# Optimization experiments

Measured on AMD Instinct MI355X. Metric: run time of the kernel, lower is better.

Reference implementation:

```python
import jax, jax.numpy as jnp
import numpy as np

E, S, B, D, F = 8, 2048, 4, 1024, 4096  # experts, seq, batch, d_model, d_ff


def setup_inputs() -> dict:
    key = jax.random.key(0)
    k_x, k_w1, k_w2, k_m = jax.random.split(key, 4)
    scale = 0.02
    x = jax.random.normal(k_x, (S, B, D), dtype=jnp.float32)
    W1 = jax.random.normal(k_w1, (E, D, F), dtype=jnp.float32) * scale
    b1 = jnp.zeros((E, F), dtype=jnp.float32)
    W2 = jax.random.normal(k_w2, (E, F, D), dtype=jnp.float32) * scale
    b2 = jnp.zeros((E, D), dtype=jnp.float32)
    mask = jax.random.randint(k_m, (S, B), 0, E)  # per-token expert id
    return {"x": x, "W1": W1, "b1": b1, "W2": W2, "b2": b2, "mask": mask}


def reference(x, W1, b1, W2, b2, mask):
    # Eval path of ThorFNN: dense all-expert 2-layer FFN, then per-token
    # random expert mask multiply-sum combine. Dropout is identity in eval.
    # h: [E, S, B, F]
    h = jax.nn.relu(jnp.einsum('sbd,edf->esbf', x, W1) + b1[:, None, None, :])
    # out: [E, S, B, D]
    out = jnp.einsum('esbf,efd->esbd', h, W2) + b2[:, None, None, :]
    sel = (mask[None, :, :, None] == jnp.arange(W1.shape[0])[:, None, None, None]).astype(out.dtype)
    return (out * sel).sum(axis=0)  # [S, B, D]
```

## Files before the change

kernel.cpp:

```cpp
#include <hip/hip_runtime.h>
#include <hip/hip_bf16.h>
#include <stdint.h>

#define E_   8
#define S_   2048
#define B_   4
#define D_   1024
#define F_   4096
#define NTOK (S_ * B_)
#define MAXT 72

typedef __attribute__((ext_vector_type(8))) __bf16 bf16x8;
typedef __attribute__((ext_vector_type(4))) float  f32x4;

#define WS_LIST 4096
#define WS_XB   65536
#define WS_W1T  (WS_XB + 16777216)
#define WS_W2T  WS_W1T
#define WS_H    (WS_W1T + 67108864)

__device__ __forceinline__ void gload_lds16(const void* g, void* l) {
    __builtin_amdgcn_global_load_lds(
        (const __attribute__((address_space(1))) void*)g,
        (__attribute__((address_space(3))) void*)l, 16, 0, 0);
}

__global__ void build_lists(const int* __restrict__ mask,
                            int* __restrict__ meta, int* __restrict__ list) {
    __shared__ int cnt[E_], cur[E_];
    int tid = threadIdx.x;
    if (tid < E_) cnt[tid] = 0;
    __syncthreads();
    for (int t = tid; t < NTOK; t += 256) atomicAdd(&cnt[mask[t]], 1);
    __syncthreads();
    if (tid == 0) {
        int acc = 0, nt = 0;
        for (int e = 0; e < E_; ++e) {
            meta[e] = cnt[e];
            meta[8 + e] = acc;
            cur[e] = acc;
            acc += cnt[e];
        }
        for (int e = 0; e < E_; ++e) {
            int mt = (cnt[e] + 127) >> 7;
            for (int m = 0; m < mt; ++m) meta[32 + nt++] = (e << 16) | m;
        }
        meta[16] = nt;
        for (; nt < MAXT; ++nt) meta[32 + nt] = -1;
    }
    __syncthreads();
    for (int t = tid; t < NTOK; t += 256) {
        int e = mask[t];
        int pos = atomicAdd(&cur[e], 1);
        list[pos] = t;
    }
}

__global__ void convert_x_kernel(const float* __restrict__ x,
                                 __hip_bfloat16* __restrict__ xb) {
    size_t i = ((size_t)blockIdx.x * blockDim.x + threadIdx.x) * 4;
    const float4 v = *(const float4*)(x + i);
    union { __hip_bfloat16 h[4]; uint2 u; } o;
    o.h[0] = __float2bfloat16(v.x);
    o.h[1] = __float2bfloat16(v.y);
    o.h[2] = __float2bfloat16(v.z);
    o.h[3] = __float2bfloat16(v.w);
    *(uint2*)(xb + i) = o.u;
}

__global__ void transpose_convert(const float* __restrict__ src,
                                  __hip_bfloat16* __restrict__ dst,
                                  int R, int C) {
    __shared__ float tile[32][33];
    size_t off = (size_t)blockIdx.z * R * C;
    src += off; dst += off;
    int c0 = blockIdx.x * 32, r0 = blockIdx.y * 32;
    int tx = threadIdx.x & 31, ty = threadIdx.x >> 5;
#pragma unroll
    for (int i = 0; i < 4; ++i)
        tile[ty + 8 * i][tx] = src[(size_t)(r0 + ty + 8 * i) * C + c0 + tx];
    __syncthreads();
#pragma unroll
    for (int i = 0; i < 4; ++i)
        dst[(size_t)(c0 + ty + 8 * i) * R + r0 + tx] =
            __float2bfloat16(tile[tx][ty + 8 * i]);
}

template <int KDIM, int NDIM, int LAYER>
__global__ __launch_bounds__(256, 2) void gemm_kernel(
    const uint8_t* __restrict__ Abase,
    const uint8_t* __restrict__ Wt,
    const float* __restrict__ bias,
    const int* __restrict__ meta, const int* __restrict__ list,
    __hip_bfloat16* __restrict__ Hout, float* __restrict__ Oout) {
    int te = meta[32 + blockIdx.x];
    if (te < 0) return;
    const int e = te >> 16, mt = te & 0xffff;
    const int cnt = meta[e], bse = meta[8 + e];
    const int n0 = blockIdx.y * 128;
    const int tid = threadIdx.x, wv = tid >> 6, l = tid & 63;
    const int wr = wv >> 1, wc = wv & 1;

    __shared__ __align__(16) uint8_t smem[2][32768];

    const uint8_t* WtE = Wt + (size_t)e * NDIM * KDIM * 2;

    size_t agoff[4], bgoff[4];
#pragma unroll
    for (int p = 0; p < 4; ++p) {
        int r = p * 32 + wv * 8 + (l >> 3);
        int grow = mt * 128 + r;
        int pidx = bse + (grow < cnt ? grow : cnt - 1);
        size_t arow = (LAYER == 1) ? (size_t)list[pidx] : (size_t)pidx;
        agoff[p] = arow * (KDIM * 2) + (size_t)(l & 7) * 16;
        bgoff[p] = (size_t)(n0 + r) * (KDIM * 2) + (size_t)(l & 7) * 16;
    }

    f32x4 acc[4][4] = {};

    auto stage = [&](int buf, int kt) {
        uint8_t* As = &smem[buf][0];
        uint8_t* Bs = &smem[buf][16384];
        size_t kb = (size_t)kt * 128;
#pragma unroll
        for (int p = 0; p < 4; ++p) {
            gload_lds16(Abase + agoff[p] + kb, As + (p * 32 + wv * 8) * 128);
            gload_lds16(WtE + bgoff[p] + kb, Bs + (p * 32 + wv * 8) * 128);
        }
    };

    auto compute = [&](int buf) {
        const uint8_t* As = &smem[buf][0];
        const uint8_t* Bs = &smem[buf][16384];
#pragma unroll
        for (int ks = 0; ks < 2; ++ks) {
            bf16x8 a[4], b[4];
#pragma unroll
            for (int mi = 0; mi < 4; ++mi)
                a[mi] = *(const bf16x8*)(As +
                    ((wr * 64 + mi * 16 + (l & 15)) * 64 + ks * 32 + (l >> 4) * 8) * 2);
#pragma unroll
            for (int ni = 0; ni < 4; ++ni)
                b[ni] = *(const bf16x8*)(Bs +
                    ((wc * 64 + ni * 16 + (l & 15)) * 64 + ks * 32 + (l >> 4) * 8) * 2);
#pragma unroll
            for (int mi = 0; mi < 4; ++mi)
#pragma unroll
                for (int ni = 0; ni < 4; ++ni)
                    acc[mi][ni] = __builtin_amdgcn_mfma_f32_16x16x32_bf16(
                        a[mi], b[ni], acc[mi][ni], 0, 0, 0);
        }
    };

    const int KT = KDIM / 64;
    stage(0, 0);
    __syncthreads();
    int cur = 0;
    for (int kt = 0; kt < KT - 1; ++kt) {
        stage(cur ^ 1, kt + 1);
        compute(cur);
        __syncthreads();
        cur ^= 1;
    }
    compute(cur);

#pragma unroll
    for (int mi = 0; mi < 4; ++mi) {
#pragma unroll
        for (int i = 0; i < 4; ++i) {
            int rl = wr * 64 + mi * 16 + (l >> 4) * 4 + i;
            int grow = mt * 128 + rl;
            if (grow < cnt) {
#pragma unroll
                for (int ni = 0; ni < 4; ++ni) {
                    int col = n0 + wc * 64 + ni * 16 + (l & 15);
                    float v = acc[mi][ni][i] + bias[(size_t)e * NDIM + col];
                    if (LAYER == 1) {
                        v = fmaxf(v, 0.f);
                        Hout[(size_t)(bse + grow) * NDIM + col] = __float2bfloat16(v);
                    } else {
                        int tok = list[bse + grow];
                        Oout[(size_t)tok * NDIM + col] = v;
                    }
                }
            }
        }
    }
}

extern "C" void kernel_launch(void* const* d_in, const int* in_sizes, int n_in,
                              void* d_out, int out_size, void* d_ws, size_t ws_size,
                              hipStream_t stream) {
    const float* x  = (const float*)d_in[0];
    const float* W1 = (const float*)d_in[1];
    const float* b1 = (const float*)d_in[2];
    const float* W2 = (const float*)d_in[3];
    const float* b2 = (const float*)d_in[4];
    const int* mask = (const int*)d_in[5];
    float* out = (float*)d_out;

    uint8_t* ws = (uint8_t*)d_ws;
    int* meta = (int*)ws;
    int* list = (int*)(ws + WS_LIST);
    __hip_bfloat16* xb  = (__hip_bfloat16*)(ws + WS_XB);
    __hip_bfloat16* w1t = (__hip_bfloat16*)(ws + WS_W1T);
    __hip_bfloat16* w2t = (__hip_bfloat16*)(ws + WS_W2T);
    __hip_bfloat16* H   = (__hip_bfloat16*)(ws + WS_H);

    build_lists<<<1, 256, 0, stream>>>(mask, meta, list);
    convert_x_kernel<<<NTOK * D_ / 4 / 256, 256, 0, stream>>>(x, xb);
    transpose_convert<<<dim3(F_ / 32, D_ / 32, E_), 256, 0, stream>>>(W1, w1t, D_, F_);
    gemm_kernel<D_, F_, 1><<<dim3(MAXT, F_ / 128), 256, 0, stream>>>(
        (const uint8_t*)xb, (const uint8_t*)w1t, b1, meta, list, H, nullptr);
    transpose_convert<<<dim3(D_ / 32, F_ / 32, E_), 256, 0, stream>>>(W2, w2t, F_, D_);
    gemm_kernel<F_, D_, 2><<<dim3(MAXT, D_ / 128), 256, 0, stream>>>(
        (const uint8_t*)H, (const uint8_t*)w2t, b2, meta, list, nullptr, out);
}
```

Measured before the change: 612.1 us.

## Shrink GEMM K-tile, raise occupancy, swizzle blocks per XCD, widen transpose

The GEMM now stages K in 32-element slices instead of 64, halving LDS use per block, and launch bounds go from 2 to 4 blocks per CU for higher occupancy. The 2D grid is flattened and remapped so that consecutive tiles of the same expert land on the same XCD, improving L2 reuse of weights. The weight transpose-convert uses 128-row tiles with float4 loads and 8-byte bf16 stores to cut memory transactions. The smaller K-step doubles the number of barriers per tile, and the 4-block launch bound may force register spilling with 64 accumulator floats per thread.

```diff
diff --git a/kernel.cpp b/kernel.cpp
--- a/kernel.cpp
+++ b/kernel.cpp
@@ -71,88 +71,105 @@
 __global__ void transpose_convert(const float* __restrict__ src,
                                   __hip_bfloat16* __restrict__ dst,
                                   int R, int C) {
-    __shared__ float tile[32][33];
+    __shared__ float tile[128][33];
     size_t off = (size_t)blockIdx.z * R * C;
-    src += off; dst += off;
-    int c0 = blockIdx.x * 32, r0 = blockIdx.y * 32;
-    int tx = threadIdx.x & 31, ty = threadIdx.x >> 5;
-#pragma unroll
-    for (int i = 0; i < 4; ++i)
-        tile[ty + 8 * i][tx] = src[(size_t)(r0 + ty + 8 * i) * C + c0 + tx];
-    __syncthreads();
-#pragma unroll
-    for (int i = 0; i < 4; ++i)
-        dst[(size_t)(c0 + ty + 8 * i) * R + r0 + tx] =
-            __float2bfloat16(tile[tx][ty + 8 * i]);
+    const float* s = src + off;
+    __hip_bfloat16* d = dst + off;
+    int r0 = blockIdx.y * 128, c0 = blockIdx.x * 32;
+    int t = threadIdx.x;
+    int rr = t >> 3, cc4 = (t & 7) * 4;
+#pragma unroll
+    for (int ii = 0; ii < 4; ++ii) {
+        float4 v = *(const float4*)(s + (size_t)(r0 + rr + 32 * ii) * C + c0 + cc4);
+        tile[rr + 32 * ii][cc4 + 0] = v.x;
+        tile[rr + 32 * ii][cc4 + 1] = v.y;
+        tile[rr + 32 * ii][cc4 + 2] = v.z;
+        tile[rr + 32 * ii][cc4 + 3] = v.w;
+    }
+    __syncthreads();
+    int wc = t >> 5;
+    int wr = (t & 31) * 4;
+#pragma unroll
+    for (int ii = 0; ii < 4; ++ii) {
+        int cc = wc + 8 * ii;
+        union { __hip_bfloat16 h[4]; uint2 u; } o;
+#pragma unroll
+        for (int k = 0; k < 4; ++k)
+            o.h[k] = __float2bfloat16(tile[wr + k][cc]);
+        *(uint2*)(d + (size_t)(c0 + cc) * R + r0 + wr) = o.u;
+    }
 }
 
 template <int KDIM, int NDIM, int LAYER>
-__global__ __launch_bounds__(256, 2) void gemm_kernel(
+__global__ __launch_bounds__(256, 4) void gemm_kernel(
     const uint8_t* __restrict__ Abase,
     const uint8_t* __restrict__ Wt,
     const float* __restrict__ bias,
     const int* __restrict__ meta, const int* __restrict__ list,
     __hip_bfloat16* __restrict__ Hout, float* __restrict__ Oout) {
-    int te = meta[32 + blockIdx.x];
+    constexpr int NT = NDIM / 128;
+    const int nblk = MAXT * NT;
+    int orig = blockIdx.x;
+    int q = nblk >> 3, r = nblk & 7;
+    int xcd = orig & 7, idx = orig >> 3;
+    int swz = (xcd < r ? xcd * (q + 1) : r * (q + 1) + (xcd - r) * q) + idx;
+    int te = meta[32 + swz / NT];
     if (te < 0) return;
     const int e = te >> 16, mt = te & 0xffff;
     const int cnt = meta[e], bse = meta[8 + e];
-    const int n0 = blockIdx.y * 128;
+    const int n0 = (swz % NT) * 128;
     const int tid = threadIdx.x, wv = tid >> 6, l = tid & 63;
     const int wr = wv >> 1, wc = wv & 1;
 
-    __shared__ __align__(16) uint8_t smem[2][32768];
+    __shared__ __align__(16) uint8_t smem[2][16384];
 
     const uint8_t* WtE = Wt + (size_t)e * NDIM * KDIM * 2;
 
-    size_t agoff[4], bgoff[4];
-#pragma unroll
-    for (int p = 0; p < 4; ++p) {
-        int r = p * 32 + wv * 8 + (l >> 3);
-        int grow = mt * 128 + r;
+    size_t agoff[2], bgoff[2];
+#pragma unroll
+    for (int p = 0; p < 2; ++p) {
+        int rrow = p * 64 + wv * 16 + (l >> 2);
+        int grow = mt * 128 + rrow;
         int pidx = bse + (grow < cnt ? grow : cnt - 1);
         size_t arow = (LAYER == 1) ? (size_t)list[pidx] : (size_t)pidx;
-        agoff[p] = arow * (KDIM * 2) + (size_t)(l & 7) * 16;
-        bgoff[p] = (size_t)(n0 + r) * (KDIM * 2) + (size_t)(l & 7) * 16;
+        agoff[p] = arow * (KDIM * 2) + (size_t)(l & 3) * 16;
+        bgoff[p] = (size_t)(n0 + rrow) * (KDIM * 2) + (size_t)(l & 3) * 16;
     }
 
     f32x4 acc[4][4] = {};
 
     auto stage = [&](int buf, int kt) {
         uint8_t* As = &smem[buf][0];
-        uint8_t* Bs = &smem[buf][16384];
-        size_t kb = (size_t)kt * 128;
-#pragma unroll
-        for (int p = 0; p < 4; ++p) {
-            gload_lds16(Abase + agoff[p] + kb, As + (p * 32 + wv * 8) * 128);
-            gload_lds16(WtE + bgoff[p] + kb, Bs + (p * 32 + wv * 8) * 128);
+        uint8_t* Bs = &smem[buf][8192];
+        size_t kb = (size_t)kt * 64;
+#pragma unroll
+        for (int p = 0; p < 2; ++p) {
+            gload_lds16(Abase + agoff[p] + kb, As + (p * 64 + wv * 16) * 64);
+            gload_lds16(WtE + bgoff[p] + kb, Bs + (p * 64 + wv * 16) * 64);
         }
     };
 
     auto compute = [&](int buf) {
         const uint8_t* As = &smem[buf][0];
-        const uint8_t* Bs = &smem[buf][16384];
-#pragma unroll
-        for (int ks = 0; ks < 2; ++ks) {
-            bf16x8 a[4], b[4];
-#pragma unroll
-            for (int mi = 0; mi < 4; ++mi)
-                a[mi] = *(const bf16x8*)(As +
-                    ((wr * 64 + mi * 16 + (l & 15)) * 64 + ks * 32 + (l >> 4) * 8) * 2);
+        const uint8_t* Bs = &smem[buf][8192];
+        bf16x8 a[4], b[4];
+#pragma unroll
+        for (int mi = 0; mi < 4; ++mi)
+            a[mi] = *(const bf16x8*)(As +
+                ((wr * 64 + mi * 16 + (l & 15)) * 32 + (l >> 4) * 8) * 2);
+#pragma unroll
+        for (int ni = 0; ni < 4; ++ni)
+            b[ni] = *(const bf16x8*)(Bs +
+                ((wc * 64 + ni * 16 + (l & 15)) * 32 + (l >> 4) * 8) * 2);
+#pragma unroll
+        for (int mi = 0; mi < 4; ++mi)
 #pragma unroll
             for (int ni = 0; ni < 4; ++ni)
-                b[ni] = *(const bf16x8*)(Bs +
-                    ((wc * 64 + ni * 16 + (l & 15)) * 64 + ks * 32 + (l >> 4) * 8) * 2);
-#pragma unroll
-            for (int mi = 0; mi < 4; ++mi)
-#pragma unroll
-                for (int ni = 0; ni < 4; ++ni)
-                    acc[mi][ni] = __builtin_amdgcn_mfma_f32_16x16x32_bf16(
-                        a[mi], b[ni], acc[mi][ni], 0, 0, 0);
-        }
+                acc[mi][ni] = __builtin_amdgcn_mfma_f32_16x16x32_bf16(
+                    a[mi], b[ni], acc[mi][ni], 0, 0, 0);
     };
 
-    const int KT = KDIM / 64;
+    const int KT = KDIM / 32;
     stage(0, 0);
     __syncthreads();
     int cur = 0;
@@ -209,10 +226,10 @@
 
     build_lists<<<1, 256, 0, stream>>>(mask, meta, list);
     convert_x_kernel<<<NTOK * D_ / 4 / 256, 256, 0, stream>>>(x, xb);
-    transpose_convert<<<dim3(F_ / 32, D_ / 32, E_), 256, 0, stream>>>(W1, w1t, D_, F_);
-    gemm_kernel<D_, F_, 1><<<dim3(MAXT, F_ / 128), 256, 0, stream>>>(
+    transpose_convert<<<dim3(F_ / 32, D_ / 128, E_), 256, 0, stream>>>(W1, w1t, D_, F_);
+    gemm_kernel<D_, F_, 1><<<MAXT * (F_ / 128), 256, 0, stream>>>(
         (const uint8_t*)xb, (const uint8_t*)w1t, b1, meta, list, H, nullptr);
-    transpose_convert<<<dim3(D_ / 32, F_ / 32, E_), 256, 0, stream>>>(W2, w2t, F_, D_);
-    gemm_kernel<F_, D_, 2><<<dim3(MAXT, D_ / 128), 256, 0, stream>>>(
+    transpose_convert<<<dim3(D_ / 32, F_ / 128, E_), 256, 0, stream>>>(W2, w2t, F_, D_);
+    gemm_kernel<F_, D_, 2><<<MAXT * (D_ / 128), 256, 0, stream>>>(
         (const uint8_t*)H, (const uint8_t*)w2t, b2, meta, list, nullptr, out);
 }
```

Result: faster. 568.0 us (-7.2%).
